# Performance work log

Measured on AMD Instinct MI355X. Metric: run time of the kernel, lower is better.

Reference implementation:

```python
import jax, jax.numpy as jnp
import numpy as np

IN_FEATURES = 256
EMBED = 512
HEADS = 8
HEAD_DIM = EMBED // HEADS
BLOCKS = 2
FFN = 2048
CLASSES = 1000
NWIRES = 8
BATCH = 8
SEQ = 2048


def _posenc(seq, dim, dtype):
    pos = jnp.arange(seq, dtype=jnp.float32)[:, None]
    div = jnp.exp(jnp.arange(0, dim, 2, dtype=jnp.float32) * (-jnp.log(10000.0) / dim))
    pe = jnp.zeros((seq, dim), dtype=jnp.float32)
    pe = pe.at[:, 0::2].set(jnp.sin(pos * div))
    pe = pe.at[:, 1::2].set(jnp.cos(pos * div))
    return pe.astype(dtype)


def _layer_norm(x, g, b, eps=1e-5):
    mu = jnp.mean(x, axis=-1, keepdims=True)
    var = jnp.var(x, axis=-1, keepdims=True)
    return (x - mu) * jax.lax.rsqrt(var + eps) * g + b


def setup_inputs() -> dict:
    key = jax.random.key(0)
    ks = jax.random.split(key, 20)
    s = 0.02
    inp = {
        'x': jax.random.normal(ks[0], (BATCH, SEQ, IN_FEATURES), dtype=jnp.float32),
        'Wi': jax.random.normal(ks[1], (EMBED, IN_FEATURES), dtype=jnp.float32) * s,
        'bi': jnp.zeros((EMBED,), dtype=jnp.float32),
        'theta_a': jax.random.normal(ks[2], (BLOCKS, NWIRES), dtype=jnp.float32),
        'Wproj': jax.random.normal(ks[3], (BLOCKS, EMBED, NWIRES), dtype=jnp.float32) * s,
        'Wq': jax.random.normal(ks[4], (BLOCKS, EMBED, EMBED), dtype=jnp.float32) * s,
        'Wk': jax.random.normal(ks[5], (BLOCKS, EMBED, EMBED), dtype=jnp.float32) * s,
        'Wv': jax.random.normal(ks[6], (BLOCKS, EMBED, EMBED), dtype=jnp.float32) * s,
        'Wo': jax.random.normal(ks[7], (BLOCKS, EMBED, EMBED), dtype=jnp.float32) * s,
        'g1': jnp.ones((BLOCKS, EMBED), dtype=jnp.float32),
        'b1': jnp.zeros((BLOCKS, EMBED), dtype=jnp.float32),
        'phi': jax.random.normal(ks[8], (BLOCKS, NWIRES), dtype=jnp.float32),
        'W1': jax.random.normal(ks[9], (BLOCKS, FFN, NWIRES), dtype=jnp.float32) * s,
        'W2': jax.random.normal(ks[10], (BLOCKS, EMBED, FFN), dtype=jnp.float32) * s,
        'g2': jnp.ones((BLOCKS, EMBED), dtype=jnp.float32),
        'b2': jnp.zeros((BLOCKS, EMBED), dtype=jnp.float32),
        'Wc': jax.random.normal(ks[11], (CLASSES, EMBED), dtype=jnp.float32) * s,
        'bc': jnp.zeros((CLASSES,), dtype=jnp.float32),
    }
    return inp


def reference(x, Wi, bi, theta_a, Wproj, Wq, Wk, Wv, Wo, g1, b1, phi, W1, W2, g2, b2, Wc, bc):
    b, s, _ = x.shape
    h = jnp.einsum('bsf,ef->bse', x, Wi) + bi          # input_proj
    h = h + _posenc(s, EMBED, h.dtype)[None]           # positional encoding
    scale = 1.0 / np.sqrt(HEAD_DIM)
    for l in range(BLOCKS):
        # --- quantum attention sublayer ---
        # RX encode first NWIRES features + trainable RX per wire -> <Z> = cos(x + theta)
        q_out = jnp.cos(h[..., :NWIRES] + theta_a[l])  # [b,s,nw]
        x_q = jnp.einsum('bsw,ew->bse', q_out, Wproj[l])
        q = jnp.einsum('bse,fe->bsf', x_q, Wq[l]).reshape(b, s, HEADS, HEAD_DIM).transpose(0, 2, 1, 3)
        k = jnp.einsum('bse,fe->bsf', x_q, Wk[l]).reshape(b, s, HEADS, HEAD_DIM).transpose(0, 2, 1, 3)
        v = jnp.einsum('bse,fe->bsf', x_q, Wv[l]).reshape(b, s, HEADS, HEAD_DIM).transpose(0, 2, 1, 3)
        scores = jnp.einsum('bhqd,bhkd->bhqk', q, k) * scale
        attn = jax.nn.softmax(scores, axis=-1)
        out = jnp.einsum('bhqk,bhkd->bhqd', attn, v)
        out = out.transpose(0, 2, 1, 3).reshape(b, s, EMBED)
        attn_out = jnp.einsum('bse,fe->bsf', out, Wo[l])
        h = _layer_norm(h + attn_out, g1[l], b1[l])
        # --- quantum feed-forward sublayer ---
        # RY encode + trainable RY per wire -> <Z> = cos(x + phi)
        qf = jnp.cos(h[..., :NWIRES] + phi[l])         # [b,s,nw]
        f = jnp.einsum('bsw,fw->bsf', qf, W1[l])       # nw -> ffn
        f = jnp.einsum('bsf,ef->bse', jax.nn.relu(f), W2[l])
        h = _layer_norm(h + f, g2[l], b2[l])
    pooled = jnp.mean(h, axis=1)                        # [b, embed]
    logits = jnp.einsum('be,ce->bc', pooled, Wc) + bc
    return logits
```

## Files before the change

### kernel.cpp

```cpp
#include <hip/hip_runtime.h>
#include <hip/hip_bf16.h>
#include <math.h>

#define B_   8
#define S_   2048
#define T_   (B_*S_)
#define FIN  256
#define E_   512
#define H_   8
#define D_   64
#define FFN_ 2048
#define NC_  1000
#define NW_  8

typedef __attribute__((ext_vector_type(8))) short short8;
typedef __attribute__((ext_vector_type(4))) short short4v;
typedef __attribute__((ext_vector_type(4))) float f32x4;

__device__ __forceinline__ unsigned short f2bf(float f) {
    __hip_bfloat16 h = __float2bfloat16(f);
    return __builtin_bit_cast(unsigned short, h);
}
__device__ __forceinline__ float bf2f(unsigned short u) {
    return __builtin_bit_cast(float, (unsigned int)u << 16);
}

__device__ __forceinline__ void gld16(void* l, const void* g) {
    __builtin_amdgcn_global_load_lds(
        (const __attribute__((address_space(1))) unsigned int*)g,
        (__attribute__((address_space(3))) unsigned int*)l,
        16, 0, 0);
}

#if defined(__has_builtin)
#if __has_builtin(__builtin_amdgcn_mfma_f32_16x16x16bf16_1k)
#define HAVE_MFMA16 1
#endif
#endif

__device__ __forceinline__ f32x4 mfma16(short4v a, short4v b, f32x4 c) {
#ifdef HAVE_MFMA16
    return __builtin_amdgcn_mfma_f32_16x16x16bf16_1k(a, b, c, 0, 0, 0);
#else
    short8 a8 = {a[0], a[1], a[2], a[3], 0, 0, 0, 0};
    short8 b8 = {b[0], b[1], b[2], b[3], 0, 0, 0, 0};
    return __builtin_amdgcn_mfma_f32_16x16x32_bf16(a8, b8, c, 0, 0, 0);
#endif
}

__global__ __launch_bounds__(256)
void cvt_all(const float* __restrict__ x,  const float* __restrict__ Wi,
             const float* __restrict__ Wo, const float* __restrict__ W2,
             const float* __restrict__ W1,
             unsigned short* xb, unsigned short* Wib,
             unsigned short* Wob, unsigned short* W2b, unsigned short* W1b)
{
    int g = blockIdx.x*256 + threadIdx.x;
    const float* s; unsigned short* d; int o;
    if      (g < 1048576) { s = x;  d = xb;  o = g; }
    else if (g < 1081344) { s = Wi; d = Wib; o = g - 1048576; }
    else if (g < 1212416) { s = Wo; d = Wob; o = g - 1081344; }
    else if (g < 1736704) { s = W2; d = W2b; o = g - 1212416; }
    else                  { s = W1; d = W1b; o = g - 1736704; }
    float4 vv = ((const float4*)s)[o];
    ushort4 u;
    u.x = f2bf(vv.x); u.y = f2bf(vv.y); u.z = f2bf(vv.z); u.w = f2bf(vv.w);
    ((ushort4*)d)[o] = u;
}

__global__ __launch_bounds__(64)
void weff_kernel(const float* __restrict__ Wq, const float* __restrict__ Wk,
                 const float* __restrict__ Wv, const float* __restrict__ Wproj,
                 unsigned short* __restrict__ Weff)
{
    const int f = blockIdx.x, l = blockIdx.y, which = blockIdx.z;
    const int lane = threadIdx.x;
    const float* W = (which == 0 ? Wq : which == 1 ? Wk : Wv)
                     + (size_t)l*E_*E_ + (size_t)f*E_;
    const float* P = Wproj + (size_t)l*E_*NW_;
    const int wv = lane & 7;
    float s = 0.f;
    for (int e = (lane >> 3)*64; e < (lane >> 3)*64 + 64; e++)
        s += W[e] * P[e*NW_ + wv];
    #pragma unroll
    for (int off = 8; off < 64; off <<= 1) s += __shfl_xor(s, off);
    const float scale = (which == 0) ? 0.18033688011112042f : 1.f;
    if (lane < 8)
        Weff[((size_t)(which*2 + l)*E_ + f)*NW_ + lane] = f2bf(s * scale);
}

__global__ __launch_bounds__(256)
void qkv_small(const unsigned short* __restrict__ h, const float* __restrict__ theta,
               const unsigned short* __restrict__ Wq_e,
               const unsigned short* __restrict__ Wk_e,
               const unsigned short* __restrict__ Wv_e,
               unsigned short* __restrict__ qo, unsigned short* __restrict__ ko,
               unsigned short* __restrict__ vT)
{
    const int tid = threadIdx.x;
    const int t0 = blockIdx.x * 32;
    __shared__ float cs[32][8];
    {
        int tl = tid >> 3, wv2 = tid & 7;
        cs[tl][wv2] = cosf(bf2f(h[(size_t)(t0 + tl)*E_ + wv2]) + theta[wv2]);
    }
    __syncthreads();
    const int f = tid * 2;
    float wq[16], wk[16], wv_[16];
    #pragma unroll
    for (int i = 0; i < 16; i++) {
        wq[i]  = bf2f(Wq_e[(size_t)f*NW_ + i]);
        wk[i]  = bf2f(Wk_e[(size_t)f*NW_ + i]);
        wv_[i] = bf2f(Wv_e[(size_t)f*NW_ + i]);
    }
    unsigned int v0p[16] __attribute__((aligned(16)));
    unsigned int v1p[16] __attribute__((aligned(16)));
    for (int t = 0; t < 32; t++) {
        float4 c01 = *(const float4*)&cs[t][0];
        float4 c23 = *(const float4*)&cs[t][4];
        float c[8] = {c01.x,c01.y,c01.z,c01.w,c23.x,c23.y,c23.z,c23.w};
        float q0=0,q1=0,k0=0,k1=0,v0=0,v1=0;
        #pragma unroll
        for (int i = 0; i < 8; i++) {
            q0 += c[i]*wq[i];  q1 += c[i]*wq[8+i];
            k0 += c[i]*wk[i];  k1 += c[i]*wk[8+i];
            v0 += c[i]*wv_[i]; v1 += c[i]*wv_[8+i];
        }
        size_t base = (size_t)(t0 + t)*E_ + f;
        ushort2 uq; uq.x = f2bf(q0); uq.y = f2bf(q1);
        ushort2 uk; uk.x = f2bf(k0); uk.y = f2bf(k1);
        *(ushort2*)&qo[base] = uq;
        *(ushort2*)&ko[base] = uk;
        unsigned int b0 = f2bf(v0), b1 = f2bf(v1);
        if (t & 1) { v0p[t>>1] |= b0 << 16; v1p[t>>1] |= b1 << 16; }
        else       { v0p[t>>1]  = b0;       v1p[t>>1]  = b1; }
    }
    const int bb = t0 >> 11, s0 = t0 & (S_ - 1);
    const int head = f >> 6, d = f & 63;
    unsigned short* r0 = vT + ((size_t)(bb*H_ + head)*64 + d)*S_ + s0;
    #pragma unroll
    for (int c = 0; c < 4; c++) *(float4*)(r0 + c*8) = *(float4*)&v0p[c*4];
    r0 += S_;
    #pragma unroll
    for (int c = 0; c < 4; c++) *(float4*)(r0 + c*8) = *(float4*)&v1p[c*4];
}

template<int TC_BF16, int MODE>
__global__ __launch_bounds__(256)
void gemm_mfma(const unsigned short* __restrict__ A,
               const unsigned short* __restrict__ Bm,
               void* __restrict__ Cv, int M, int N, int K,
               float scale, const float* __restrict__ bias)
{
    __shared__ unsigned short Al[2][128*32];
    __shared__ unsigned short Bl[2][128*32];
    const int tid  = threadIdx.x;
    const int lane = tid & 63;
    const int w    = tid >> 6;
    const int wx   = w & 1, wy = w >> 1;
    int bx, by;
    {
        int nx = gridDim.x;
        int bid = blockIdx.y * nx + blockIdx.x;
        int rpx = gridDim.y >> 3;
        int xcd = bid & 7, idx = bid >> 3;
        by = xcd * rpx + idx / nx;
        bx = idx % nx;
    }
    const int rowBase = by * 128;
    const int colBase = bx * 128;
    const int l15  = lane & 15;
    const int quad = lane >> 4;
    const int srow = lane >> 2;
    const int gch  = (lane & 3) ^ ((srow >> 1) & 3);
    const int swz  = (l15 >> 1) & 3;

    f32x4 acc[4][4] = {};

    #pragma unroll
    for (int it = 0; it < 2; it++) {
        int rb = it*64 + w*16;
        gld16(&Al[0][rb*32], A  + (size_t)(rowBase + rb + srow)*K + gch*8);
        gld16(&Bl[0][rb*32], Bm + (size_t)(colBase + rb + srow)*K + gch*8);
    }

    for (int k0 = 0; k0 < K; k0 += 32) {
        const int cur = (k0 >> 5) & 1;
        __syncthreads();
        if (k0 + 32 < K) {
            #pragma unroll
            for (int it = 0; it < 2; it++) {
                int rb = it*64 + w*16;
                gld16(&Al[1-cur][rb*32], A  + (size_t)(rowBase + rb + srow)*K + k0 + 32 + gch*8);
                gld16(&Bl[1-cur][rb*32], Bm + (size_t)(colBase + rb + srow)*K + k0 + 32 + gch*8);
            }
        }
        short8 af[4], bfr[4];
        #pragma unroll
        for (int mi = 0; mi < 4; mi++)
            af[mi] = *(const short8*)&Al[cur][(wy*64 + mi*16 + l15)*32 + ((quad ^ swz) << 3)];
        #pragma unroll
        for (int ni = 0; ni < 4; ni++)
            bfr[ni] = *(const short8*)&Bl[cur][(wx*64 + ni*16 + l15)*32 + ((quad ^ swz) << 3)];
        #pragma unroll
        for (int mi = 0; mi < 4; mi++)
            #pragma unroll
            for (int ni = 0; ni < 4; ni++)
                acc[mi][ni] = __builtin_amdgcn_mfma_f32_16x16x32_bf16(
                    af[mi], bfr[ni], acc[mi][ni], 0, 0, 0);
    }

    #pragma unroll
    for (int mi = 0; mi < 4; mi++) {
        #pragma unroll
        for (int ni = 0; ni < 4; ni++) {
            #pragma unroll
            for (int r = 0; r < 4; r++) {
                int row = rowBase + wy*64 + mi*16 + quad*4 + r;
                int col = colBase + wx*64 + ni*16 + l15;
                float v = acc[mi][ni][r] * scale;
                if (MODE == 1) {
                    int s = row & (S_ - 1);
                    float freq = __expf(-0.017988946039244957f * (float)(col & ~1));
                    float ang = (float)s * freq;
                    v += bias[col] + ((col & 1) ? cosf(ang) : sinf(ang));
                }
                if (TC_BF16) ((unsigned short*)Cv)[(size_t)row*N + col] = f2bf(v);
                else         ((float*)Cv)[(size_t)row*N + col] = v;
            }
        }
    }
}

__global__ __launch_bounds__(256)
void gemm_w2f(const unsigned short* __restrict__ h, const float* __restrict__ phi,
              const unsigned short* __restrict__ W1b,
              const unsigned short* __restrict__ W2b,
              unsigned short* __restrict__ tmp)
{
    __shared__ char Lraw[17408];
    unsigned short* Wl = (unsigned short*)Lraw;
    float* Ot = (float*)Lraw;

    const int tid  = threadIdx.x;
    const int lane = tid & 63;
    const int w    = tid >> 6;
    const int tx   = w & 1, ty = w >> 1;
    const int l15  = lane & 15;
    const int quad = lane >> 4;
    const int srow = lane >> 2;
    const int gch  = (lane & 3) ^ ((srow >> 1) & 3);
    const int swz  = (l15 >> 1) & 3;

    const int bid = blockIdx.x;
    const int xcd = bid & 7;
    const int eb  = xcd >> 1;
    const int tb  = (xcd & 1) * 64 + (bid >> 3);
    const int tBase = tb * 128;
    const int eBase = eb * 128;

    short4v cosfr[4];
    #pragma unroll
    for (int nt = 0; nt < 4; nt++) {
        short4v c = {0,0,0,0};
        if (quad < 2) {
            int tok = tBase + ty*64 + nt*16 + l15;
            #pragma unroll
            for (int i = 0; i < 4; i++) {
                int wv = quad*4 + i;
                c[i] = (short)f2bf(cosf(bf2f(h[(size_t)tok*E_ + wv]) + phi[wv]));
            }
        }
        cosfr[nt] = c;
    }

    #pragma unroll
    for (int it = 0; it < 2; it++) {
        int rb = w*32 + it*16;
        gld16(&Wl[rb*32], W2b + (size_t)(eBase + rb + srow)*FFN_ + gch*8);
    }
    short4v w1f[2] = {{0,0,0,0},{0,0,0,0}};
    #pragma unroll
    for (int jb = 0; jb < 2; jb++)
        if (quad < 2)
            w1f[jb] = *(const short4v*)&W1b[(size_t)(jb*16 + l15)*NW_ + quad*4];

    f32x4 acc[4][4] = {};
    const f32x4 fzero = {0.f, 0.f, 0.f, 0.f};

    for (int k0 = 0; k0 < FFN_; k0 += 32) {
        const int cur = (k0 >> 5) & 1;
        __syncthreads();
        if (k0 + 32 < FFN_) {
            #pragma unroll
            for (int it = 0; it < 2; it++) {
                int rb = w*32 + it*16;
                gld16(&Wl[(1-cur)*4096 + rb*32],
                      W2b + (size_t)(eBase + rb + srow)*FFN_ + k0 + 32 + gch*8);
            }
        }
        short4v pf[4][2];
        #pragma unroll
        for (int nt = 0; nt < 4; nt++)
            #pragma unroll
            for (int jb = 0; jb < 2; jb++) {
                f32x4 c = mfma16(w1f[jb], cosfr[nt], fzero);
                short4v p;
                #pragma unroll
                for (int r = 0; r < 4; r++)
                    p[r] = (short)f2bf(fmaxf(c[r], 0.f));
                pf[nt][jb] = p;
            }
        if (k0 + 32 < FFN_) {
            #pragma unroll
            for (int jb = 0; jb < 2; jb++)
                if (quad < 2)
                    w1f[jb] = *(const short4v*)&W1b[(size_t)(k0 + 32 + jb*16 + l15)*NW_ + quad*4];
        }
        #pragma unroll
        for (int et = 0; et < 4; et++)
            #pragma unroll
            for (int jb = 0; jb < 2; jb++) {
                short4v wf = *(const short4v*)&Wl[cur*4096 + (tx*64 + et*16 + l15)*32
                               + (((jb*2 + (quad>>1)) ^ swz) << 3) + (quad & 1)*4];
                #pragma unroll
                for (int nt = 0; nt < 4; nt++)
                    acc[et][nt] = mfma16(wf, pf[nt][jb], acc[et][nt]);
            }
    }

    #pragma unroll
    for (int et = 0; et < 4; et++) {
        __syncthreads();
        #pragma unroll
        for (int nt = 0; nt < 4; nt++)
            #pragma unroll
            for (int r = 0; r < 4; r++)
                Ot[(ty*64 + nt*16 + l15)*33 + tx*16 + quad*4 + r] = acc[et][nt][r];
        __syncthreads();
        int token = tid >> 1, half = tid & 1;
        unsigned short u[16] __attribute__((aligned(16)));
        #pragma unroll
        for (int i = 0; i < 16; i++) u[i] = f2bf(Ot[token*33 + half*16 + i]);
        unsigned short* dst = tmp + (size_t)(tBase + token)*E_ + eBase + half*64 + et*16;
        *(float4*)dst       = *(float4*)&u[0];
        *(float4*)(dst + 8) = *(float4*)&u[8];
    }
}

__global__ __launch_bounds__(256)
void flash_attn(const unsigned short* __restrict__ q,
                const unsigned short* __restrict__ k,
                const unsigned short* __restrict__ vT,
                unsigned short* __restrict__ o)
{
    __shared__ unsigned short L[17168];
    unsigned short* Ks = L;
    unsigned short* Vt = L + 8192;
    float* Ot = (float*)L;

    const int tid  = threadIdx.x;
    const int lane = tid & 63;
    const int w    = tid >> 6;
    const int l15  = lane & 15;
    const int quad = lane >> 4;
    const int bid  = blockIdx.x;
    const int xcd  = bid & 7;
    const int rest = bid >> 3;
    const int combo = xcd * 8 + (rest >> 4);
    const int qt = rest & 15;
    const int hh = combo & 7;
    const int bb = combo >> 3;
    const size_t qrow0 = (size_t)bb*S_ + (size_t)qt*128;
    const unsigned short* qp  = q  + qrow0*E_ + hh*64;
    const unsigned short* kp  = k  + ((size_t)bb*S_)*E_ + hh*64;
    const unsigned short* vtp = vT + (size_t)(bb*H_ + hh)*64*S_;

    const int srow8 = lane >> 3;
    const int gch8  = (lane & 7) ^ srow8;
    const int sql   = l15 & 7;

    #pragma unroll
    for (int it = 0; it < 4; it++) {
        int rb = it*32 + w*8;
        gld16(&L[rb*64], qp + (size_t)(rb + srow8)*E_ + gch8*8);
    }
    __syncthreads();
    short8 qfr[2][2];
    #pragma unroll
    for (int mi = 0; mi < 2; mi++)
        #pragma unroll
        for (int kc = 0; kc < 2; kc++)
            qfr[mi][kc] = *(const short8*)&L[(w*32 + mi*16 + l15)*64
                                             + (((kc*4 + quad) ^ sql) << 3)];
    __syncthreads();

    #pragma unroll
    for (int it = 0; it < 2; it++) {
        int rb = it*32 + w*8;
        gld16(&Ks[rb*64], kp  + (size_t)(rb + srow8)*E_ + gch8*8);
        gld16(&Vt[rb*64], vtp + (size_t)(rb + srow8)*S_ + gch8*8);
    }

    const short4v ones = {(short)0x3F80, (short)0x3F80, (short)0x3F80, (short)0x3F80};
    f32x4 O[2][4] = {};
    f32x4 Ol[2]   = {};

    for (int kt = 0; kt < S_/64; kt++) {
        const int cur = kt & 1;
        __syncthreads();
        if (kt + 1 < S_/64) {
            #pragma unroll
            for (int it = 0; it < 2; it++) {
                int rb = it*32 + w*8;
                gld16(&Ks[(1-cur)*4096 + rb*64],
                      kp  + (size_t)((kt+1)*64 + rb + srow8)*E_ + gch8*8);
                gld16(&Vt[(1-cur)*4096 + rb*64],
                      vtp + (size_t)(rb + srow8)*S_ + (kt+1)*64 + gch8*8);
            }
        }
        f32x4 Sc[2][4] = {};
        #pragma unroll
        for (int kc = 0; kc < 2; kc++)
            #pragma unroll
            for (int nt = 0; nt < 4; nt++) {
                short8 kf = *(const short8*)&Ks[cur*4096 + (nt*16 + l15)*64
                                                 + (((kc*4 + quad) ^ sql) << 3)];
                Sc[0][nt] = __builtin_amdgcn_mfma_f32_16x16x32_bf16(kf, qfr[0][kc], Sc[0][nt], 0, 0, 0);
                Sc[1][nt] = __builtin_amdgcn_mfma_f32_16x16x32_bf16(kf, qfr[1][kc], Sc[1][nt], 0, 0, 0);
            }
        short4v pf[2][4];
        #pragma unroll
        for (int mi = 0; mi < 2; mi++)
            #pragma unroll
            for (int nt = 0; nt < 4; nt++) {
                short4v pv;
                pv[0] = (short)f2bf(__builtin_amdgcn_exp2f(Sc[mi][nt][0]));
                pv[1] = (short)f2bf(__builtin_amdgcn_exp2f(Sc[mi][nt][1]));
                pv[2] = (short)f2bf(__builtin_amdgcn_exp2f(Sc[mi][nt][2]));
                pv[3] = (short)f2bf(__builtin_amdgcn_exp2f(Sc[mi][nt][3]));
                pf[mi][nt] = pv;
                Ol[mi] = mfma16(ones, pv, Ol[mi]);
            }
        #pragma unroll
        for (int dt = 0; dt < 4; dt++)
            #pragma unroll
            for (int nt = 0; nt < 4; nt++) {
                short4v vf = *(const short4v*)&Vt[cur*4096 + (dt*16 + l15)*64
                               + (((nt*2 + (quad >> 1)) ^ sql) << 3) + (quad & 1)*4];
                O[0][dt] = mfma16(vf, pf[0][nt], O[0][dt]);
                O[1][dt] = mfma16(vf, pf[1][nt], O[1][dt]);
            }
    }

    __syncthreads();
    #pragma unroll
    for (int mi = 0; mi < 2; mi++) {
        float inv = 1.f / Ol[mi][0];
        #pragma unroll
        for (int dt = 0; dt < 4; dt++)
            #pragma unroll
            for (int r = 0; r < 4; r++)
                Ot[(w*32 + mi*16 + l15)*67 + dt*16 + quad*4 + r] = O[mi][dt][r] * inv;
    }
    __syncthreads();
    {
        int row = tid >> 1, half = tid & 1;
        unsigned short u[32] __attribute__((aligned(16)));
        #pragma unroll
        for (int i = 0; i < 32; i++) u[i] = f2bf(Ot[row*67 + half*32 + i]);
        unsigned short* dst = o + (qrow0 + row)*E_ + hh*64 + half*32;
        #pragma unroll
        for (int c = 0; c < 4; c++) *(float4*)(dst + c*8) = *(float4*)&u[c*8];
    }
}

__global__ __launch_bounds__(256)
void add_ln(unsigned short* __restrict__ h, const unsigned short* __restrict__ delta,
            const float* __restrict__ g, const float* __restrict__ b)
{
    const int lane = threadIdx.x & 63;
    const int t = blockIdx.x*4 + (threadIdx.x >> 6);
    const size_t base = (size_t)t*E_ + lane*8;
    uint4 hv = *(const uint4*)&h[base];
    uint4 dv = *(const uint4*)&delta[base];
    float x[8];
    #pragma unroll
    for (int i = 0; i < 4; i++) {
        unsigned hu = ((const unsigned*)&hv)[i], du = ((const unsigned*)&dv)[i];
        x[2*i]   = bf2f((unsigned short)(hu & 0xffff)) + bf2f((unsigned short)(du & 0xffff));
        x[2*i+1] = bf2f((unsigned short)(hu >> 16))    + bf2f((unsigned short)(du >> 16));
    }
    float s = 0.f, sq = 0.f;
    #pragma unroll
    for (int i = 0; i < 8; i++) { s += x[i]; sq += x[i]*x[i]; }
    #pragma unroll
    for (int off = 1; off < 64; off <<= 1) {
        s  += __shfl_xor(s,  off);
        sq += __shfl_xor(sq, off);
    }
    float mu  = s * (1.f/E_);
    float var = sq * (1.f/E_) - mu*mu;
    float rstd = rsqrtf(var + 1e-5f);
    float4 g0 = *(const float4*)&g[lane*8], g1 = *(const float4*)&g[lane*8 + 4];
    float4 b0 = *(const float4*)&b[lane*8], b1 = *(const float4*)&b[lane*8 + 4];
    float gg[8] = {g0.x,g0.y,g0.z,g0.w,g1.x,g1.y,g1.z,g1.w};
    float bb[8] = {b0.x,b0.y,b0.z,b0.w,b1.x,b1.y,b1.z,b1.w};
    uint4 ov;
    #pragma unroll
    for (int i = 0; i < 4; i++) {
        unsigned lo = f2bf((x[2*i]   - mu)*rstd*gg[2*i]   + bb[2*i]);
        unsigned hi = f2bf((x[2*i+1] - mu)*rstd*gg[2*i+1] + bb[2*i+1]);
        ((unsigned*)&ov)[i] = lo | (hi << 16);
    }
    *(uint4*)&h[base] = ov;
}

__global__ __launch_bounds__(256)
void pool_partial(const unsigned short* __restrict__ h, float* __restrict__ part)
{
    const int chunk = blockIdx.x, bb = blockIdx.y, tid = threadIdx.x;
    for (int e = tid; e < E_; e += 256) {
        const unsigned short* p = h + ((size_t)bb*S_ + (size_t)chunk*128)*E_ + e;
        float s = 0.f;
        for (int r = 0; r < 128; r++) s += bf2f(p[(size_t)r*E_]);
        part[(size_t)(bb*16 + chunk)*E_ + e] = s;
    }
}

__global__ __launch_bounds__(256)
void pool_final(const float* __restrict__ part, float* __restrict__ pooled)
{
    const int bb = blockIdx.x, tid = threadIdx.x;
    for (int e = tid; e < E_; e += 256) {
        float s = 0.f;
        #pragma unroll
        for (int c = 0; c < 16; c++) s += part[(size_t)(bb*16 + c)*E_ + e];
        pooled[bb*E_ + e] = s * (1.f/S_);
    }
}

__global__ __launch_bounds__(64)
void classify(const float* __restrict__ pooled, const float* __restrict__ Wc,
              const float* __restrict__ bc, float* __restrict__ out)
{
    const int c = blockIdx.x, bb = blockIdx.y, lane = threadIdx.x;
    const float* p = pooled + bb*E_;
    const float* wc = Wc + (size_t)c*E_;
    float s = 0.f;
    for (int e = lane; e < E_; e += 64) s += p[e]*wc[e];
    #pragma unroll
    for (int off = 1; off < 64; off <<= 1) s += __shfl_xor(s, off);
    if (lane == 0) out[bb*NC_ + c] = s + bc[c];
}

extern "C" void kernel_launch(void* const* d_in, const int* in_sizes, int n_in,
                              void* d_out, int out_size, void* d_ws, size_t ws_size,
                              hipStream_t stream)
{
    const float* x       = (const float*)d_in[0];
    const float* Wi      = (const float*)d_in[1];
    const float* bi      = (const float*)d_in[2];
    const float* theta_a = (const float*)d_in[3];
    const float* Wproj   = (const float*)d_in[4];
    const float* Wq      = (const float*)d_in[5];
    const float* Wk      = (const float*)d_in[6];
    const float* Wv      = (const float*)d_in[7];
    const float* Wo      = (const float*)d_in[8];
    const float* g1      = (const float*)d_in[9];
    const float* b1      = (const float*)d_in[10];
    const float* phi     = (const float*)d_in[11];
    const float* W1      = (const float*)d_in[12];
    const float* W2      = (const float*)d_in[13];
    const float* g2      = (const float*)d_in[14];
    const float* b2      = (const float*)d_in[15];
    const float* Wc      = (const float*)d_in[16];
    const float* bc      = (const float*)d_in[17];
    float* out = (float*)d_out;

    char* ws = (char*)d_ws;
    const size_t MB = 1024u*1024u;
    unsigned short* h      = (unsigned short*)(ws + 0*MB);
    unsigned short* tmp    = (unsigned short*)(ws + 16*MB);
    unsigned short* qb     = (unsigned short*)(ws + 32*MB);
    unsigned short* kb     = (unsigned short*)(ws + 48*MB);
    unsigned short* vT     = (unsigned short*)(ws + 64*MB);
    unsigned short* ao     = (unsigned short*)(ws + 80*MB);
    unsigned short* xb     = (unsigned short*)(ws + 96*MB);
    unsigned short* Wib    = (unsigned short*)(ws + 104*MB);
    unsigned short* Wob    = (unsigned short*)(ws + 105*MB);
    unsigned short* W2b    = (unsigned short*)(ws + 106*MB);
    unsigned short* W1b    = (unsigned short*)(ws + 110*MB);
    unsigned short* Weff   = (unsigned short*)(ws + 111*MB);
    float*          part   = (float*)(ws + 112*MB);
    float*          pooled = (float*)(ws + 112*MB + 512*1024);

    cvt_all<<<6816, 256, 0, stream>>>(x, Wi, Wo, W2, W1, xb, Wib, Wob, W2b, W1b);
    weff_kernel<<<dim3(E_, 2, 3), 64, 0, stream>>>(Wq, Wk, Wv, Wproj, Weff);

    gemm_mfma<1,1><<<dim3(E_/128, T_/128), 256, 0, stream>>>(
        xb, Wib, h, T_, E_, FIN, 1.f, bi);

    for (int l = 0; l < 2; l++) {
        const unsigned short* Wq_e = Weff + (size_t)(0*2 + l)*E_*NW_;
        const unsigned short* Wk_e = Weff + (size_t)(1*2 + l)*E_*NW_;
        const unsigned short* Wv_e = Weff + (size_t)(2*2 + l)*E_*NW_;
        qkv_small<<<T_/32, 256, 0, stream>>>(h, theta_a + l*NW_, Wq_e, Wk_e, Wv_e, qb, kb, vT);
        flash_attn<<<(S_/128)*H_*B_, 256, 0, stream>>>(qb, kb, vT, ao);
        gemm_mfma<1,0><<<dim3(E_/128, T_/128), 256, 0, stream>>>(
            ao, Wob + (size_t)l*E_*E_, tmp, T_, E_, E_, 1.f, nullptr);
        add_ln<<<T_/4, 256, 0, stream>>>(h, tmp, g1 + l*E_, b1 + l*E_);

        gemm_w2f<<<512, 256, 0, stream>>>(h, phi + l*NW_,
                                          W1b + (size_t)l*FFN_*NW_,
                                          W2b + (size_t)l*E_*FFN_, tmp);
        add_ln<<<T_/4, 256, 0, stream>>>(h, tmp, g2 + l*E_, b2 + l*E_);
    }

    pool_partial<<<dim3(16, B_), 256, 0, stream>>>(h, part);
    pool_final<<<B_, 256, 0, stream>>>(part, pooled);
    classify<<<dim3(NC_, B_), 64, 0, stream>>>(pooled, Wc, bc, out);
}
```

Measured before the change: 691.8 us.

## Process two K/V tiles per barrier and sum softmax denominators with shuffles

The flash-attention loop now stages two 64-key K/V tiles per iteration in a doubled shared-memory buffer, which halves the number of barriers and lengthens the prefetch distance. The row-sum of exponentials is now accumulated in fp32 registers and reduced across lanes with shuffles, replacing the extra MFMA against a ones vector. Score computation is split per query sub-tile to lower register pressure. The cost is twice the LDS per block, which may reduce occupancy, and a denominator summed from unrounded fp32 values rather than the bf16-rounded ones.

```diff
diff --git a/kernel.cpp b/kernel.cpp
--- a/kernel.cpp
+++ b/kernel.cpp
@@ -354,9 +354,9 @@
                 const unsigned short* __restrict__ vT,
                 unsigned short* __restrict__ o)
 {
-    __shared__ unsigned short L[17168];
+    __shared__ unsigned short L[32768];
     unsigned short* Ks = L;
-    unsigned short* Vt = L + 8192;
+    unsigned short* Vt = L + 16384;
     float* Ot = (float*)L;
 
     const int tid  = threadIdx.x;
@@ -396,67 +396,80 @@
     __syncthreads();
 
     #pragma unroll
-    for (int it = 0; it < 2; it++) {
-        int rb = it*32 + w*8;
-        gld16(&Ks[rb*64], kp  + (size_t)(rb + srow8)*E_ + gch8*8);
-        gld16(&Vt[rb*64], vtp + (size_t)(rb + srow8)*S_ + gch8*8);
-    }
-
-    const short4v ones = {(short)0x3F80, (short)0x3F80, (short)0x3F80, (short)0x3F80};
+    for (int t2 = 0; t2 < 2; t2++)
+        #pragma unroll
+        for (int it = 0; it < 2; it++) {
+            int rb = it*32 + w*8;
+            gld16(&Ks[t2*4096 + rb*64], kp  + (size_t)(t2*64 + rb + srow8)*E_ + gch8*8);
+            gld16(&Vt[t2*4096 + rb*64], vtp + (size_t)(rb + srow8)*S_ + t2*64 + gch8*8);
+        }
+
+    float lsum[2] = {0.f, 0.f};
     f32x4 O[2][4] = {};
-    f32x4 Ol[2]   = {};
-
-    for (int kt = 0; kt < S_/64; kt++) {
-        const int cur = kt & 1;
+
+    for (int kp2 = 0; kp2 < S_/128; kp2++) {
+        const int cur = kp2 & 1;
         __syncthreads();
-        if (kt + 1 < S_/64) {
-            #pragma unroll
-            for (int it = 0; it < 2; it++) {
-                int rb = it*32 + w*8;
-                gld16(&Ks[(1-cur)*4096 + rb*64],
-                      kp  + (size_t)((kt+1)*64 + rb + srow8)*E_ + gch8*8);
-                gld16(&Vt[(1-cur)*4096 + rb*64],
-                      vtp + (size_t)(rb + srow8)*S_ + (kt+1)*64 + gch8*8);
+        if (kp2 + 1 < S_/128) {
+            #pragma unroll
+            for (int t2 = 0; t2 < 2; t2++)
+                #pragma unroll
+                for (int it = 0; it < 2; it++) {
+                    int rb = it*32 + w*8;
+                    gld16(&Ks[((1-cur)*2 + t2)*4096 + rb*64],
+                          kp  + (size_t)((kp2+1)*128 + t2*64 + rb + srow8)*E_ + gch8*8);
+                    gld16(&Vt[((1-cur)*2 + t2)*4096 + rb*64],
+                          vtp + (size_t)(rb + srow8)*S_ + (kp2+1)*128 + t2*64 + gch8*8);
+                }
+        }
+        #pragma unroll
+        for (int t2 = 0; t2 < 2; t2++) {
+            const int ts = (cur*2 + t2)*4096;
+            #pragma unroll
+            for (int mi = 0; mi < 2; mi++) {
+                f32x4 Sc[4] = {};
+                #pragma unroll
+                for (int kc = 0; kc < 2; kc++)
+                    #pragma unroll
+                    for (int nt = 0; nt < 4; nt++) {
+                        short8 kf = *(const short8*)&Ks[ts + (nt*16 + l15)*64
+                                                         + (((kc*4 + quad) ^ sql) << 3)];
+                        Sc[nt] = __builtin_amdgcn_mfma_f32_16x16x32_bf16(kf, qfr[mi][kc], Sc[nt], 0, 0, 0);
+                    }
+                short4v pf[4];
+                #pragma unroll
+                for (int nt = 0; nt < 4; nt++) {
+                    float p0 = __builtin_amdgcn_exp2f(Sc[nt][0]);
+                    float p1 = __builtin_amdgcn_exp2f(Sc[nt][1]);
+                    float p2 = __builtin_amdgcn_exp2f(Sc[nt][2]);
+                    float p3 = __builtin_amdgcn_exp2f(Sc[nt][3]);
+                    lsum[mi] += (p0 + p1) + (p2 + p3);
+                    short4v pv;
+                    pv[0] = (short)f2bf(p0); pv[1] = (short)f2bf(p1);
+                    pv[2] = (short)f2bf(p2); pv[3] = (short)f2bf(p3);
+                    pf[nt] = pv;
+                }
+                #pragma unroll
+                for (int dt = 0; dt < 4; dt++)
+                    #pragma unroll
+                    for (int nt = 0; nt < 4; nt++) {
+                        short4v vf = *(const short4v*)&Vt[ts + (dt*16 + l15)*64
+                                       + (((nt*2 + (quad >> 1)) ^ sql) << 3) + (quad & 1)*4];
+                        O[mi][dt] = mfma16(vf, pf[nt], O[mi][dt]);
+                    }
             }
         }
-        f32x4 Sc[2][4] = {};
-        #pragma unroll
-        for (int kc = 0; kc < 2; kc++)
-            #pragma unroll
-            for (int nt = 0; nt < 4; nt++) {
-                short8 kf = *(const short8*)&Ks[cur*4096 + (nt*16 + l15)*64
-                                                 + (((kc*4 + quad) ^ sql) << 3)];
-                Sc[0][nt] = __builtin_amdgcn_mfma_f32_16x16x32_bf16(kf, qfr[0][kc], Sc[0][nt], 0, 0, 0);
-                Sc[1][nt] = __builtin_amdgcn_mfma_f32_16x16x32_bf16(kf, qfr[1][kc], Sc[1][nt], 0, 0, 0);
-            }
-        short4v pf[2][4];
-        #pragma unroll
-        for (int mi = 0; mi < 2; mi++)
-            #pragma unroll
-            for (int nt = 0; nt < 4; nt++) {
-                short4v pv;
-                pv[0] = (short)f2bf(__builtin_amdgcn_exp2f(Sc[mi][nt][0]));
-                pv[1] = (short)f2bf(__builtin_amdgcn_exp2f(Sc[mi][nt][1]));
-                pv[2] = (short)f2bf(__builtin_amdgcn_exp2f(Sc[mi][nt][2]));
-                pv[3] = (short)f2bf(__builtin_amdgcn_exp2f(Sc[mi][nt][3]));
-                pf[mi][nt] = pv;
-                Ol[mi] = mfma16(ones, pv, Ol[mi]);
-            }
-        #pragma unroll
-        for (int dt = 0; dt < 4; dt++)
-            #pragma unroll
-            for (int nt = 0; nt < 4; nt++) {
-                short4v vf = *(const short4v*)&Vt[cur*4096 + (dt*16 + l15)*64
-                               + (((nt*2 + (quad >> 1)) ^ sql) << 3) + (quad & 1)*4];
-                O[0][dt] = mfma16(vf, pf[0][nt], O[0][dt]);
-                O[1][dt] = mfma16(vf, pf[1][nt], O[1][dt]);
-            }
-    }
-
+    }
+
+    #pragma unroll
+    for (int mi = 0; mi < 2; mi++) {
+        lsum[mi] += __shfl_xor(lsum[mi], 16);
+        lsum[mi] += __shfl_xor(lsum[mi], 32);
+    }
     __syncthreads();
     #pragma unroll
     for (int mi = 0; mi < 2; mi++) {
-        float inv = 1.f / Ol[mi][0];
+        float inv = 1.f / lsum[mi];
         #pragma unroll
         for (int dt = 0; dt < 4; dt++)
             #pragma unroll
```

Measured after the change: 710.0 us. 1.03x slower.
